# Optimization experiments

Hardware: AMD Instinct MI355X
Metric: run time of the kernel (lower is better)

The kernel has to match this reference:

```python
import jax, jax.numpy as jnp
import numpy as np

N = 4096
NODE_DIM = 256
HIDDEN = 64
N_CLASSES = 16
N_HEADS = 4
NEG_SLOPE = 0.01  # F.leaky_relu default


def _xavier(key, shape):
    fan_out, fan_in = shape[0], shape[1]
    limit = float(np.sqrt(6.0 / (fan_in + fan_out)))
    return jax.random.uniform(key, shape, jnp.float32, -limit, limit)


def setup_inputs() -> dict:
    key = jax.random.key(0)
    ks = jax.random.split(key, 8)
    x = jax.random.normal(ks[0], (N, NODE_DIM), jnp.float32)
    adj_mat = jax.random.randint(ks[1], (N, N), 0, 2, jnp.int32)
    # head-stacked layer-1 params
    W1 = _xavier(ks[2], (N_HEADS * HIDDEN, NODE_DIM)).reshape(N_HEADS, HIDDEN, NODE_DIM)
    a1_1 = _xavier(ks[3], (N_HEADS * HIDDEN, 1)).reshape(N_HEADS, HIDDEN)
    a2_1 = _xavier(ks[4], (N_HEADS * HIDDEN, 1)).reshape(N_HEADS, HIDDEN)
    # layer-2 params
    W2 = _xavier(ks[5], (N_CLASSES, N_HEADS * HIDDEN))
    a1_2 = _xavier(ks[6], (N_CLASSES, 1))[:, 0]
    a2_2 = _xavier(ks[7], (N_CLASSES, 1))[:, 0]
    return {"x": x, "adj_mat": adj_mat, "W1": W1, "a1_1": a1_1, "a2_1": a2_1,
            "W2": W2, "a1_2": a1_2, "a2_2": a2_2}


def _attention_layer(x, adj_f, W, a1, a2):
    # x: [N, in_dim], W: [out_dim, in_dim], a1/a2: [out_dim]
    h = x @ W.T                               # [N, d]
    f1 = h @ a1                               # [N]
    f2 = h @ a2                               # [N]
    e = jax.nn.leaky_relu(f1[:, None] + f2[None, :], NEG_SLOPE)  # [N, N]
    e = e * adj_f
    e = jnp.where(e == 0, -jnp.inf, e)        # faithful to torch.where(e==0, -inf, e)
    alpha = jax.nn.softmax(e, axis=1)         # [N, N]
    return alpha @ h                          # [N, d]


def reference(x, adj_mat, W1, a1_1, a2_1, W2, a1_2, a2_2):
    adj_f = adj_mat.astype(x.dtype)
    # layer 1: vmap over heads, concat along feature dim
    heads = jax.vmap(_attention_layer, in_axes=(None, None, 0, 0, 0))(
        x, adj_f, W1, a1_1, a2_1)              # [H, N, hidden]
    h = jnp.transpose(heads, (1, 0, 2)).reshape(N, N_HEADS * HIDDEN)
    h = jax.nn.elu(h)
    # dropout p=0.0 -> identity
    logits = _attention_layer(h, adj_f, W2, a1_2, a2_2)  # [N, n_classes]
    return logits
```

## Files before the change

### kernel.cpp

```cpp
#include <hip/hip_runtime.h>
#include <cstdint>

typedef __bf16 bf16x8 __attribute__((ext_vector_type(8)));
typedef float  f32x4  __attribute__((ext_vector_type(4)));

#define LOG2E 1.4426950408889634f
#define LGKM0 do { asm volatile("s_waitcnt lgkmcnt(0)" ::: "memory"); \
                   __builtin_amdgcn_sched_barrier(0); } while (0)

__device__ __forceinline__ void split8(const float* v, bf16x8& hi, bf16x8& lo) {
    union { bf16x8 v; __bf16 e[8]; } h, l;
    #pragma unroll
    for (int j = 0; j < 8; j++) {
        __bf16 hb = (__bf16)v[j];
        float  r  = v[j] - (float)hb;
        h.e[j] = hb; l.e[j] = (__bf16)r;
    }
    hi = h.v; lo = l.v;
}
__device__ __forceinline__ bf16x8 cvt8(const float* v) {
    union { bf16x8 v; __bf16 e[8]; } u;
    #pragma unroll
    for (int j = 0; j < 8; j++) u.e[j] = (__bf16)v[j];
    return u.v;
}
__device__ __forceinline__ void splitstore(unsigned short* ph, unsigned short* pl, float v) {
    __bf16 hb = (__bf16)v;
    float  r  = v - (float)hb;
    __bf16 lb = (__bf16)r;
    unsigned short hu, lu;
    __builtin_memcpy(&hu, &hb, 2); __builtin_memcpy(&lu, &lb, 2);
    *ph = hu; *pl = lu;
}
__device__ __forceinline__ unsigned short f2bfh(float v) {
    __bf16 hb = (__bf16)v; unsigned short hu;
    __builtin_memcpy(&hu, &hb, 2); return hu;
}

__global__ __launch_bounds__(256)
void kzero(float4* __restrict__ p) {
    p[blockIdx.x * 256 + threadIdx.x] = float4{0.f, 0.f, 0.f, 0.f};
}

__global__ __launch_bounds__(256)
void kpre2(const int* __restrict__ adj, unsigned long long* __restrict__ bm64,
           const float* __restrict__ x, const float* __restrict__ w1,
           const float* __restrict__ a11, const float* __restrict__ a21,
           unsigned short* __restrict__ h1t_hi, float* __restrict__ fvals) {
    int bx = blockIdx.x, tid = threadIdx.x;
    if (bx < 256) {
        int wave = tid >> 6, lane = tid & 63;
        int q = lane >> 4, m = lane & 15;
        int i0 = bx * 16;
        int c0 = wave * 64;
        f32x4 acc[4] = {};
        #pragma unroll
        for (int k0 = 0; k0 < 256; k0 += 32) {
            bf16x8 ah, al;
            split8(x + (i0 + m) * 256 + k0 + q * 8, ah, al);
            #pragma unroll
            for (int ct = 0; ct < 4; ct++) {
                bf16x8 bh, bl;
                split8(w1 + (c0 + ct * 16 + m) * 256 + k0 + q * 8, bh, bl);
                acc[ct] = __builtin_amdgcn_mfma_f32_16x16x32_bf16(ah, bh, acc[ct], 0, 0, 0);
                acc[ct] = __builtin_amdgcn_mfma_f32_16x16x32_bf16(al, bh, acc[ct], 0, 0, 0);
                acc[ct] = __builtin_amdgcn_mfma_f32_16x16x32_bf16(ah, bl, acc[ct], 0, 0, 0);
            }
        }
        float a1v[4], a2v[4];
        #pragma unroll
        for (int ct = 0; ct < 4; ct++) {
            a1v[ct] = a11[wave * 64 + ct * 16 + m];
            a2v[ct] = a21[wave * 64 + ct * 16 + m];
        }
        #pragma unroll
        for (int r = 0; r < 4; r++) {
            int i = i0 + q * 4 + r;
            float s1 = 0.f, s2 = 0.f;
            #pragma unroll
            for (int ct = 0; ct < 4; ct++) {
                int c = c0 + ct * 16 + m;
                h1t_hi[c * 4096 + i] = f2bfh(acc[ct][r]);
                s1 += acc[ct][r] * a1v[ct];
                s2 += acc[ct][r] * a2v[ct];
            }
            #pragma unroll
            for (int off = 1; off < 16; off <<= 1) {
                s1 += __shfl_xor(s1, off);
                s2 += __shfl_xor(s2, off);
            }
            if (m == 0) {
                fvals[wave * 4096 + i] = s1 * LOG2E;
                fvals[16384 + wave * 4096 + i] = s2 * LOG2E;
            }
        }
        return;
    }
    int bxa = bx - 256;
    int row = bxa >> 1, jbase = (bxa & 1) * 2048;
    int wave = tid >> 6, lane = tid & 63;
    const int* base = adj + (size_t)row * 4096 + jbase + wave * 512;
    unsigned long long* bmw = bm64 + row * 64 + (jbase >> 6) + wave * 8;
    #pragma unroll
    for (int it = 0; it < 8; it++) {
        int v = base[it * 64 + lane];
        unsigned long long mask = __ballot(v != 0);
        if (lane == 0) bmw[it] = mask;
    }
}

template<int NCT, int JLEN, bool ATOM>
__global__ __launch_bounds__(256)
void attn_kernel(const unsigned char* __restrict__ bmb,
                 const float* __restrict__ f1_all,
                 const float* __restrict__ f2_all,
                 const unsigned short* __restrict__ BTh_all,
                 float* __restrict__ pacc,
                 float* __restrict__ zacc,
                 int pstride) {
    constexpr int S    = JLEN / 32;
    constexpr int ST   = (S % 8 == 0) ? S + 4 : S;
    constexpr int PR   = S / 4;
    constexpr int R    = 64;
    constexpr int NU4  = R * PR;
    constexpr int CR   = NCT * 16;
    constexpr int TSTR = 72;
    constexpr int NIT  = JLEN / 64;
    constexpr int BUFO = CR * TSTR;
    int tid = threadIdx.x, wave = tid >> 6, lane = tid & 63;
    int q = lane >> 4, m = lane & 15;
    int head = blockIdx.y;
    int i0 = blockIdx.x * R;
    int jstart = blockIdx.z * JLEN;

    if (!ATOM) {
        pacc += (size_t)blockIdx.z * (size_t)(4096 * pstride);
        zacc += (size_t)blockIdx.z * (size_t)((NCT == 4 ? 4 : 1) * 4096);
    }

    __shared__ unsigned int ldsbm[R * ST];
    __shared__ unsigned short ldsbt[2][BUFO];
    __shared__ float ldsf2[JLEN];

    const unsigned short* BTh = BTh_all + (size_t)head * CR * 4096;
    const float* f1 = f1_all + head * 4096;
    const float* f2 = f2_all + head * 4096;

    for (int c = tid; c < NU4; c += 256) {
        int row = c / PR, part = c % PR;
        uint4 v = *(const uint4*)(bmb + (size_t)(i0 + row) * 512 + (jstart >> 3) + part * 16);
        *(uint4*)&ldsbm[row * ST + part * 4] = v;
    }
    for (int c = tid; c < JLEN / 4; c += 256)
        *(float4*)&ldsf2[c * 4] = *(const float4*)(f2 + jstart + c * 4);

    int sc = tid >> 2, sp = tid & 3;
    bool stager = (NCT == 4) ? true : (tid < CR * 4);
    const unsigned short* sbase = BTh + (size_t)sc * 4096 + jstart + sp * 8;
    unsigned short* swr0 = &ldsbt[0][0] + sc * TSTR + sp * 8;

    uint4 vA0, vA1, vB0, vB1;
    if (stager) {
        uint4 t00 = *(const uint4*)(sbase);
        uint4 t01 = *(const uint4*)(sbase + 32);
        *(uint4*)(swr0) = t00;
        *(uint4*)(swr0 + 32) = t01;
        vB0 = *(const uint4*)(sbase + 64);
        vB1 = *(const uint4*)(sbase + 96);
    }

    int col0 = head * CR;
    int r0 = wave * 16;
    float f1s0 = f1[i0 + r0 + m];

    f32x4 acc0[NCT] = {};
    float z0 = 0.f;
    int mrow = (r0 + m) * ST;

    auto compute = [&](int it, int cur) {
        int jl = it * 64;
        unsigned long long mw = *(const unsigned long long*)&ldsbm[mrow + 2 * it];
        const unsigned short* rb = &ldsbt[0][0] + cur * BUFO;
        #pragma unroll
        for (int js = 0; js < 2; js++) {
            unsigned int md0 = (js == 0) ? (unsigned int)mw : (unsigned int)(mw >> 32);
            const float4* f2p = (const float4*)&ldsf2[jl + js * 32 + q * 8];
            float4 fa = f2p[0], fb = f2p[1];
            float fv[8] = {fa.x, fa.y, fa.z, fa.w, fb.x, fb.y, fb.z, fb.w};
            float pv0[8];
            #pragma unroll
            for (int jj = 0; jj < 8; jj++) {
                int bit = q * 8 + jj;
                float s0 = f1s0 + fv[jj];
                float e0 = fmaxf(s0, 0.01f * s0);
                bool v0 = ((md0 >> bit) & 1u) && (s0 != 0.0f);
                float p0 = v0 ? __builtin_amdgcn_exp2f(e0) : 0.0f;
                z0 += p0; pv0[jj] = p0;
            }
            bf16x8 ah0 = cvt8(pv0);
            #pragma unroll
            for (int ct = 0; ct < NCT; ct++) {
                bf16x8 bh = *(const bf16x8*)(rb + (ct * 16 + m) * TSTR + js * 32 + q * 8);
                acc0[ct] = __builtin_amdgcn_mfma_f32_16x16x32_bf16(ah0, bh, acc0[ct], 0, 0, 0);
            }
        }
    };

    LGKM0;
    for (int itp = 0; itp + 2 < NIT; itp += 2) {
        __builtin_amdgcn_s_barrier();
        if (stager) {
            vA0 = *(const uint4*)(sbase + (itp + 2) * 64);
            vA1 = *(const uint4*)(sbase + (itp + 2) * 64 + 32);
        }
        compute(itp, 0);
        if (stager) {
            *(uint4*)(swr0 + BUFO) = vB0;
            *(uint4*)(swr0 + BUFO + 32) = vB1;
        }
        LGKM0;
        __builtin_amdgcn_s_barrier();
        if (stager) {
            vB0 = *(const uint4*)(sbase + (itp + 3) * 64);
            vB1 = *(const uint4*)(sbase + (itp + 3) * 64 + 32);
        }
        compute(itp + 1, 1);
        if (stager) {
            *(uint4*)(swr0) = vA0;
            *(uint4*)(swr0 + 32) = vA1;
        }
        LGKM0;
    }
    __builtin_amdgcn_s_barrier();
    compute(NIT - 2, 0);
    if (stager) {
        *(uint4*)(swr0 + BUFO) = vB0;
        *(uint4*)(swr0 + BUFO + 32) = vB1;
    }
    LGKM0;
    __builtin_amdgcn_s_barrier();
    compute(NIT - 1, 1);

    z0 += __shfl_xor(z0, 16); z0 += __shfl_xor(z0, 32);
    if (lane < 16) {
        if (ATOM) {
            atomicAdd(&zacc[head * 4096 + i0 + r0 + lane], z0);
        } else {
            zacc[head * 4096 + i0 + r0 + lane] = z0;
        }
    }
    #pragma unroll
    for (int ct = 0; ct < NCT; ct++)
        #pragma unroll
        for (int r = 0; r < 4; r++) {
            int col = col0 + ct * 16 + m;
            int rowA = i0 + r0 + q * 4 + r;
            if (ATOM) {
                atomicAdd(&pacc[rowA * pstride + col], acc0[ct][r]);
            } else {
                pacc[rowA * pstride + col] = acc0[ct][r];
            }
        }
}

__global__ __launch_bounds__(256)
void fin1c(const float* __restrict__ pp, const float* __restrict__ zp, int nj,
           unsigned short* __restrict__ hh, unsigned short* __restrict__ hl) {
    int row = blockIdx.x, col = threadIdx.x;
    float s = 0.f;
    for (int jc = 0; jc < nj; jc++) s += pp[(size_t)jc * (4096 * 256) + row * 256 + col];
    int head = col >> 6;
    float zz = 0.f;
    for (int jc = 0; jc < nj; jc++) zz += zp[jc * (4 * 4096) + head * 4096 + row];
    float v = s / zz;
    v = (v > 0.f) ? v : (__expf(v) - 1.0f);
    splitstore(&hh[row * 256 + col], &hl[row * 256 + col], v);
}

__global__ __launch_bounds__(256)
void k3_layer2(const unsigned short* __restrict__ helu_hi,
               const unsigned short* __restrict__ helu_lo,
               const float* __restrict__ w2,
               const float* __restrict__ a12,
               const float* __restrict__ a22,
               unsigned short* __restrict__ h2t_hi,
               float* __restrict__ fq) {
    int tid = threadIdx.x, wave = tid >> 6, lane = tid & 63;
    int q = lane >> 4, m = lane & 15;
    int i0 = (blockIdx.x * 4 + wave) * 16;
    f32x4 acc = {};
    #pragma unroll
    for (int k0 = 0; k0 < 256; k0 += 32) {
        bf16x8 ah = *(const bf16x8*)(helu_hi + (i0 + m) * 256 + k0 + q * 8);
        bf16x8 al = *(const bf16x8*)(helu_lo + (i0 + m) * 256 + k0 + q * 8);
        bf16x8 bh, bl;
        split8(w2 + m * 256 + k0 + q * 8, bh, bl);
        acc = __builtin_amdgcn_mfma_f32_16x16x32_bf16(ah, bh, acc, 0, 0, 0);
        acc = __builtin_amdgcn_mfma_f32_16x16x32_bf16(al, bh, acc, 0, 0, 0);
        acc = __builtin_amdgcn_mfma_f32_16x16x32_bf16(ah, bl, acc, 0, 0, 0);
    }
    float a1v = a12[m], a2v = a22[m];
    #pragma unroll
    for (int r = 0; r < 4; r++) {
        float v = acc[r];
        int i = i0 + q * 4 + r;
        h2t_hi[m * 4096 + i] = f2bfh(v);
        float s1 = v * a1v, s2 = v * a2v;
        #pragma unroll
        for (int off = 1; off < 16; off <<= 1) {
            s1 += __shfl_xor(s1, off);
            s2 += __shfl_xor(s2, off);
        }
        if (m == 0) { fq[i] = s1 * LOG2E; fq[4096 + i] = s2 * LOG2E; }
    }
}

__global__ __launch_bounds__(256)
void fin2(const float* __restrict__ pp, const float* __restrict__ zp, int nj,
          float* __restrict__ out) {
    int idx = blockIdx.x * 256 + threadIdx.x;
    float s = 0.f;
    for (int jc = 0; jc < nj; jc++) s += pp[jc * 65536 + idx];
    float zz = 0.f;
    for (int jc = 0; jc < nj; jc++) zz += zp[jc * 4096 + (idx >> 4)];
    out[idx] = s / zz;
}

extern "C" void kernel_launch(void* const* d_in, const int* in_sizes, int n_in,
                              void* d_out, int out_size, void* d_ws, size_t ws_size,
                              hipStream_t stream) {
    const float* x   = (const float*)d_in[0];
    const int*   adj = (const int*)d_in[1];
    const float* w1  = (const float*)d_in[2];
    const float* a11 = (const float*)d_in[3];
    const float* a21 = (const float*)d_in[4];
    const float* w2  = (const float*)d_in[5];
    const float* a12 = (const float*)d_in[6];
    const float* a22 = (const float*)d_in[7];
    float* out = (float*)d_out;

    uint8_t* w = (uint8_t*)d_ws;
    unsigned long long* bm  = (unsigned long long*)(w);
    unsigned short* h1t_hi  = (unsigned short*)(w + (2u << 20));
    unsigned short* h2t_hi  = (unsigned short*)(w + (4u << 20));
    float*          fvals   = (float*)(w + (4u << 20) + (128u << 10));
    float*          fq      = (float*)(w + (4u << 20) + (256u << 10));
    unsigned short* helu_hi = (unsigned short*)(w + (4u << 20) + (560u << 10));
    unsigned short* helu_lo = (unsigned short*)(w + (4u << 20) + (2608u << 10));

    bool big = ws_size >= ((size_t)48 << 20);
    float* p1 = (float*)(w + (9u << 20));
    float *z1, *p2, *z2;
    if (big) {
        z1 = p1 + (size_t)4 * 4096 * 256;
        p2 = z1 + 4 * 4 * 4096;
        z2 = p2 + (size_t)16 * 4096 * 16;
    } else {
        z1 = p1 + 4096 * 256;
        p2 = z1 + 4 * 4096;
        z2 = p2 + 4096 * 16;
    }

    if (!big) kzero<<<1108, 256, 0, stream>>>((float4*)p1);
    kpre2<<<8448, 256, 0, stream>>>(adj, bm, x, w1, a11, a21, h1t_hi, fvals);
    if (big)
        attn_kernel<4, 1024, false><<<dim3(64, 4, 4), 256, 0, stream>>>(
            (const unsigned char*)bm, fvals, fvals + 16384, h1t_hi, p1, z1, 256);
    else
        attn_kernel<4, 1024, true><<<dim3(64, 4, 4), 256, 0, stream>>>(
            (const unsigned char*)bm, fvals, fvals + 16384, h1t_hi, p1, z1, 256);
    fin1c<<<4096, 256, 0, stream>>>(p1, z1, big ? 4 : 1, helu_hi, helu_lo);
    k3_layer2<<<64, 256, 0, stream>>>(helu_hi, helu_lo, w2, a12, a22,
                                      h2t_hi, fq);
    if (big)
        attn_kernel<1, 256, false><<<dim3(64, 1, 16), 256, 0, stream>>>(
            (const unsigned char*)bm, fq, fq + 4096, h2t_hi, p2, z2, 16);
    else
        attn_kernel<1, 256, true><<<dim3(64, 1, 16), 256, 0, stream>>>(
            (const unsigned char*)bm, fq, fq + 4096, h2t_hi, p2, z2, 16);
    fin2<<<256, 256, 0, stream>>>(p2, z2, big ? 16 : 1, out);
}
```

Before: 182.9 us.

## Fuse layer-1 finalize with layer-2 projection and split softmax-sum accumulators

Merges the layer-1 normalization/ELU kernel with the layer-2 linear projection. Each block normalizes 16 rows into LDS and feeds them straight into the MFMA matmul, so the bf16 hi/lo ELU intermediate is no longer written to and re-read from global memory, and one launch is removed. The attention kernel also spreads the softmax denominator over four partial accumulators to shorten the serial add chain. The risk is that the fused kernel runs only 256 blocks and only one wave does the MFMA part, so parallelism is lower.

```diff
diff --git a/kernel.cpp b/kernel.cpp
--- a/kernel.cpp
+++ b/kernel.cpp
@@ -23,14 +23,6 @@
     #pragma unroll
     for (int j = 0; j < 8; j++) u.e[j] = (__bf16)v[j];
     return u.v;
-}
-__device__ __forceinline__ void splitstore(unsigned short* ph, unsigned short* pl, float v) {
-    __bf16 hb = (__bf16)v;
-    float  r  = v - (float)hb;
-    __bf16 lb = (__bf16)r;
-    unsigned short hu, lu;
-    __builtin_memcpy(&hu, &hb, 2); __builtin_memcpy(&lu, &lb, 2);
-    *ph = hu; *pl = lu;
 }
 __device__ __forceinline__ unsigned short f2bfh(float v) {
     __bf16 hb = (__bf16)v; unsigned short hu;
@@ -174,7 +166,7 @@
     float f1s0 = f1[i0 + r0 + m];
 
     f32x4 acc0[NCT] = {};
-    float z0 = 0.f;
+    float zp[4] = {0.f, 0.f, 0.f, 0.f};
     int mrow = (r0 + m) * ST;
 
     auto compute = [&](int it, int cur) {
@@ -195,7 +187,7 @@
                 float e0 = fmaxf(s0, 0.01f * s0);
                 bool v0 = ((md0 >> bit) & 1u) && (s0 != 0.0f);
                 float p0 = v0 ? __builtin_amdgcn_exp2f(e0) : 0.0f;
-                z0 += p0; pv0[jj] = p0;
+                zp[jj & 3] += p0; pv0[jj] = p0;
             }
             bf16x8 ah0 = cvt8(pv0);
             #pragma unroll
@@ -241,6 +233,7 @@
     __builtin_amdgcn_s_barrier();
     compute(NIT - 1, 1);
 
+    float z0 = (zp[0] + zp[1]) + (zp[2] + zp[3]);
     z0 += __shfl_xor(z0, 16); z0 += __shfl_xor(z0, 32);
     if (lane < 16) {
         if (ATOM) {
@@ -264,35 +257,40 @@
 }
 
 __global__ __launch_bounds__(256)
-void fin1c(const float* __restrict__ pp, const float* __restrict__ zp, int nj,
-           unsigned short* __restrict__ hh, unsigned short* __restrict__ hl) {
-    int row = blockIdx.x, col = threadIdx.x;
-    float s = 0.f;
-    for (int jc = 0; jc < nj; jc++) s += pp[(size_t)jc * (4096 * 256) + row * 256 + col];
-    int head = col >> 6;
-    float zz = 0.f;
-    for (int jc = 0; jc < nj; jc++) zz += zp[jc * (4 * 4096) + head * 4096 + row];
-    float v = s / zz;
-    v = (v > 0.f) ? v : (__expf(v) - 1.0f);
-    splitstore(&hh[row * 256 + col], &hl[row * 256 + col], v);
-}
-
-__global__ __launch_bounds__(256)
-void k3_layer2(const unsigned short* __restrict__ helu_hi,
-               const unsigned short* __restrict__ helu_lo,
-               const float* __restrict__ w2,
-               const float* __restrict__ a12,
-               const float* __restrict__ a22,
-               unsigned short* __restrict__ h2t_hi,
-               float* __restrict__ fq) {
-    int tid = threadIdx.x, wave = tid >> 6, lane = tid & 63;
-    int q = lane >> 4, m = lane & 15;
-    int i0 = (blockIdx.x * 4 + wave) * 16;
+void fin1k3(const float* __restrict__ pp, const float* __restrict__ zp, int nj,
+            const float* __restrict__ w2,
+            const float* __restrict__ a12, const float* __restrict__ a22,
+            unsigned short* __restrict__ h2t_hi, float* __restrict__ fq) {
+    __shared__ float ldsh[16][260];
+    __shared__ float ldszz[64];
+    int tid = threadIdx.x;
+    int i0 = blockIdx.x * 16;
+    if (tid < 64) {
+        int r = tid >> 2, h = tid & 3;
+        float zz = 0.f;
+        for (int jc = 0; jc < nj; jc++) zz += zp[jc * (4 * 4096) + h * 4096 + i0 + r];
+        ldszz[r * 4 + h] = zz;
+    }
+    __syncthreads();
+    int col = tid;
+    int hd = col >> 6;
+    #pragma unroll 4
+    for (int r = 0; r < 16; r++) {
+        float s = 0.f;
+        for (int jc = 0; jc < nj; jc++)
+            s += pp[(size_t)jc * (4096 * 256) + (size_t)(i0 + r) * 256 + col];
+        float v = s / ldszz[r * 4 + hd];
+        v = (v > 0.f) ? v : (__expf(v) - 1.0f);
+        ldsh[r][col] = v;
+    }
+    __syncthreads();
+    if (tid >= 64) return;
+    int lane = tid, q = lane >> 4, m = lane & 15;
     f32x4 acc = {};
     #pragma unroll
     for (int k0 = 0; k0 < 256; k0 += 32) {
-        bf16x8 ah = *(const bf16x8*)(helu_hi + (i0 + m) * 256 + k0 + q * 8);
-        bf16x8 al = *(const bf16x8*)(helu_lo + (i0 + m) * 256 + k0 + q * 8);
+        bf16x8 ah, al;
+        split8(&ldsh[m][k0 + q * 8], ah, al);
         bf16x8 bh, bl;
         split8(w2 + m * 256 + k0 + q * 8, bh, bl);
         acc = __builtin_amdgcn_mfma_f32_16x16x32_bf16(ah, bh, acc, 0, 0, 0);
@@ -345,8 +343,6 @@
     unsigned short* h2t_hi  = (unsigned short*)(w + (4u << 20));
     float*          fvals   = (float*)(w + (4u << 20) + (128u << 10));
     float*          fq      = (float*)(w + (4u << 20) + (256u << 10));
-    unsigned short* helu_hi = (unsigned short*)(w + (4u << 20) + (560u << 10));
-    unsigned short* helu_lo = (unsigned short*)(w + (4u << 20) + (2608u << 10));
 
     bool big = ws_size >= ((size_t)48 << 20);
     float* p1 = (float*)(w + (9u << 20));
@@ -369,9 +365,8 @@
     else
         attn_kernel<4, 1024, true><<<dim3(64, 4, 4), 256, 0, stream>>>(
             (const unsigned char*)bm, fvals, fvals + 16384, h1t_hi, p1, z1, 256);
-    fin1c<<<4096, 256, 0, stream>>>(p1, z1, big ? 4 : 1, helu_hi, helu_lo);
-    k3_layer2<<<64, 256, 0, stream>>>(helu_hi, helu_lo, w2, a12, a22,
-                                      h2t_hi, fq);
+    fin1k3<<<256, 256, 0, stream>>>(p1, z1, big ? 4 : 1, w2, a12, a22,
+                                    h2t_hi, fq);
     if (big)
         attn_kernel<1, 256, false><<<dim3(64, 1, 16), 256, 0, stream>>>(
             (const unsigned char*)bm, fq, fq + 4096, h2t_hi, p2, z2, 16);
```

Result: slower. 191.2 us (+4.5%).
